# Performance work log

Measured on AMD Instinct MI355X. Metric: run time of the kernel, lower is better.

The kernel has to match this reference:

```python
import jax, jax.numpy as jnp
import numpy as np

N_NODES = 50000


def _sage_conv(x, src, dst, Wl, bl, Wr):
    # PyG SAGEConv (mean aggr): out = lin_l(mean_{j in N(i)} x_j) + lin_r(x_i)
    msgs = x[src]                                              # [E, F]
    agg = jax.ops.segment_sum(msgs, dst, num_segments=N_NODES)  # [N, F]
    cnt = jax.ops.segment_sum(jnp.ones((dst.shape[0],), x.dtype), dst,
                              num_segments=N_NODES)
    mean = agg / jnp.maximum(cnt, 1.0)[:, None]
    return mean @ Wl + bl + x @ Wr


def setup_inputs() -> dict:
    key = jax.random.key(0)
    ks = jax.random.split(key, 12)
    in_c, hid_c, out_c = 128, 128, 64
    E, P = 800000, 200000
    s = lambda k, shp: jax.random.normal(k, shp, dtype=jnp.float32) * (1.0 / np.sqrt(shp[0]))
    return {
        "x": jax.random.normal(ks[0], (N_NODES, in_c), dtype=jnp.float32),
        "edge_index": jax.random.randint(ks[1], (2, E), 0, N_NODES),
        "edge_pairs": jax.random.randint(ks[2], (2, P), 0, N_NODES),
        "W1l": s(ks[3], (in_c, hid_c)),
        "b1": jnp.zeros((hid_c,), jnp.float32),
        "W1r": s(ks[4], (in_c, hid_c)),
        "W2l": s(ks[5], (hid_c, out_c)),
        "b2": jnp.zeros((out_c,), jnp.float32),
        "W2r": s(ks[6], (hid_c, out_c)),
        "Wlin": s(ks[7], (2 * out_c, 1)),
        "blin": jnp.zeros((1,), jnp.float32),
    }


def reference(x, edge_index, edge_pairs, W1l, b1, W1r, W2l, b2, W2r, Wlin, blin):
    src, dst = edge_index[0], edge_index[1]
    h = jax.nn.relu(_sage_conv(x, src, dst, W1l, b1, W1r))
    z = _sage_conv(h, src, dst, W2l, b2, W2r)                 # [N, out_c]
    ps, pd = edge_pairs[0], edge_pairs[1]
    hcat = jnp.concatenate([z[ps], z[pd]], axis=1)            # [P, 2*out_c]
    logits = hcat @ Wlin + blin                               # [P, 1]
    return jax.nn.sigmoid(logits).reshape(-1)
```

## Files before the change

kernel.cpp:

```cpp
#include <hip/hip_runtime.h>
#include <math.h>


typedef __attribute__((ext_vector_type(8))) short bf16x8;
typedef __attribute__((ext_vector_type(4))) float f32x4;
typedef unsigned int uint32;
typedef unsigned short ushort16;

#define MAXBUCK 784
#define NHB 512

__device__ __forceinline__ ushort16 f2bf(float f) {
    uint32 u = __float_as_uint(f);
    uint32 r = u + 0x7FFFu + ((u >> 16) & 1u);
    return (ushort16)(r >> 16);
}


__global__ __launch_bounds__(256)
void prep_kernel(const float* __restrict__ x, uint32* __restrict__ xh, long long n4,
                 const float* __restrict__ W1l, const float* __restrict__ W1r,
                 ushort16* __restrict__ W1t,
                 const float* __restrict__ W2l, const float* __restrict__ W2r,
                 const float* __restrict__ Wlin, const float* __restrict__ b2,
                 float* __restrict__ fw, float* __restrict__ fc,
                 const int* __restrict__ dst, int* __restrict__ hcnt, int E,
                 int nbx, int nbw1) {
    __shared__ int lh[MAXBUCK];
    int b = blockIdx.x;
    int t = threadIdx.x;
    if (b < nbx) {
        long long i = (long long)b * 256 + t;
        if (i < n4) {
            float4 v = ((const float4*)x)[i];
            uint2 o;
            o.x = (uint32)f2bf(v.x) | ((uint32)f2bf(v.y) << 16);
            o.y = (uint32)f2bf(v.z) | ((uint32)f2bf(v.w) << 16);
            ((uint2*)xh)[i] = o;
        }
    } else if (b < nbx + nbw1) {
        int idx = (b - nbx) * 256 + t;
        int n = idx >> 8, k = idx & 255;
        float v = (k < 128) ? W1l[k * 128 + n] : W1r[(k - 128) * 128 + n];
        W1t[n * 256 + k] = f2bf(v);
    } else if (b == nbx + nbw1) {
        if (t < 128) {
            float a = 0.f, c = 0.f;
            for (int l = 0; l < 64; ++l) {
                float w = W2l[t * 64 + l];
                a += w * Wlin[l];
                c += w * Wlin[64 + l];
            }
            fw[t] = a; fw[128 + t] = c;
        } else {
            int k = t - 128;
            float a = 0.f, c = 0.f;
            for (int l = 0; l < 64; ++l) {
                float w = W2r[k * 64 + l];
                a += w * Wlin[l];
                c += w * Wlin[64 + l];
            }
            fw[256 + k] = a; fw[384 + k] = c;
        }
        if (t == 0) { float s = 0.f; for (int l = 0; l < 64; ++l) s += b2[l] * Wlin[l];      fc[0] = s; }
        if (t == 1) { float s = 0.f; for (int l = 0; l < 64; ++l) s += b2[l] * Wlin[64 + l]; fc[1] = s; }
    } else {
        int hb = b - nbx - nbw1 - 1;
        for (int i = t; i < MAXBUCK; i += 256) lh[i] = 0;
        __syncthreads();
        int per = (E + NHB - 1) / NHB;
        int e0 = hb * per, e1 = min(e0 + per, E);
        for (int e = e0 + t; e < e1; e += 256) atomicAdd(&lh[dst[e] >> 6], 1);
        __syncthreads();
        for (int i = t; i < MAXBUCK; i += 256)
            hcnt[hb * MAXBUCK + i] = lh[i];
    }
}


__global__ __launch_bounds__(256)
void offs_kernel(const int* __restrict__ hcnt, int* __restrict__ boff,
                 int* __restrict__ tot) {
    int k = blockIdx.x * 4 + (threadIdx.x >> 6);
    int lane = threadIdx.x & 63;
    if (k >= MAXBUCK) return;
    int carry = 0;
    #pragma unroll
    for (int c = 0; c < NHB / 64; ++c) {
        int hb = c * 64 + lane;
        int v = hcnt[hb * MAXBUCK + k];
        int s = v;
        #pragma unroll
        for (int off = 1; off < 64; off <<= 1) {
            int u = __shfl_up(s, off, 64);
            if (lane >= off) s += u;
        }
        boff[hb * MAXBUCK + k] = carry + s - v;
        carry += __shfl(s, 63, 64);
    }
    if (lane == 0) tot[k] = carry;
}


__global__ void bucket_scan_kernel(const int* __restrict__ tot,
                                   int* __restrict__ bbase, int nbuck) {
    __shared__ int part[256];
    int t = threadIdx.x;
    int lo = t * 4;
    int hi = min(lo + 4, nbuck);
    int loc[4];
    int s = 0;
    for (int i = lo; i < hi; ++i) { loc[i - lo] = tot[i]; s += loc[i - lo]; }
    part[t] = s;
    __syncthreads();
    for (int off = 1; off < 256; off <<= 1) {
        int v = (t >= off) ? part[t - off] : 0;
        __syncthreads();
        part[t] += v;
        __syncthreads();
    }
    int run = (t == 0) ? 0 : part[t - 1];
    for (int i = lo; i < hi; ++i) { bbase[i] = run; run += loc[i - lo]; }
    if (t == 255) bbase[nbuck] = part[255];
}


__global__ __launch_bounds__(256)
void scatter_kernel(const int* __restrict__ src, const int* __restrict__ dst,
                    const int* __restrict__ bbase, const int* __restrict__ boff,
                    uint32* __restrict__ recs, int E) {
    __shared__ int lh[MAXBUCK];
    __shared__ int lb[MAXBUCK];
    int t = threadIdx.x;
    int hb = blockIdx.x;
    int per = (E + NHB - 1) / NHB;
    int e0 = hb * per, e1 = min(e0 + per, E);
    for (int i = t; i < MAXBUCK; i += 256) {
        lh[i] = 0;
        lb[i] = bbase[i] + boff[hb * MAXBUCK + i];
    }
    __syncthreads();
    for (int e = e0 + t; e < e1; e += 256) {
        int d = dst[e];
        int b = d >> 6;
        int r = atomicAdd(&lh[b], 1);
        recs[lb[b] + r] = (uint32)src[e] | ((uint32)(d & 63) << 16);
    }
}


__global__ __launch_bounds__(256)
void sort_kernel(const uint32* __restrict__ recs, const int* __restrict__ bbase,
                 int* __restrict__ rowptr, ushort16* __restrict__ esrc,
                 int N, int E) {
    __shared__ int lh[64];
    int b = blockIdx.x;
    int t = threadIdx.x;
    int s0 = bbase[b], s1 = bbase[b + 1];
    if (t < 64) lh[t] = 0;
    __syncthreads();
    for (int i = s0 + t; i < s1; i += 256)
        atomicAdd(&lh[recs[i] >> 16], 1);
    __syncthreads();
    if (t < 64) {
        int v = lh[t];
        int incl = v;
        #pragma unroll
        for (int off = 1; off < 64; off <<= 1) {
            int u = __shfl_up(incl, off, 64);
            if (t >= off) incl += u;
        }
        int excl = incl - v;
        int node = b * 64 + t;
        if (node < N) rowptr[node] = s0 + excl;
        lh[t] = excl;
    }
    __syncthreads();
    for (int i = s0 + t; i < s1; i += 256) {
        uint32 r = recs[i];
        int pos = atomicAdd(&lh[r >> 16], 1);
        esrc[s0 + pos] = (ushort16)(r & 0xFFFFu);
    }
    if (b == 0 && t == 0) rowptr[N] = E;
}


__global__ void agg_mean_x_kernel(const uint32* __restrict__ xh,
                                  const int* __restrict__ rowptr,
                                  const ushort16* __restrict__ esrc,
                                  uint32* __restrict__ meanh, int N) {
    int node = blockIdx.x * 4 + (threadIdx.x >> 6);
    int lane = threadIdx.x & 63;
    if (node >= N) return;
    int s0 = rowptr[node], s1 = rowptr[node + 1];
    if (s0 == s1) { meanh[(size_t)node * 64 + lane] = 0u; return; }
    float ax[16] = {}, ay[16] = {};
    for (int k = s0; k < s1; k += 16) {
        int idx[16]; float msk[16];
        #pragma unroll
        for (int j = 0; j < 16; ++j) {
            int kj = k + j;
            idx[j] = esrc[kj < s1 ? kj : k];
            msk[j] = (kj < s1) ? 1.f : 0.f;
        }
        #pragma unroll
        for (int j = 0; j < 16; ++j) {
            uint32 v = xh[(size_t)idx[j] * 64 + lane];
            ax[j] += __uint_as_float(v << 16) * msk[j];
            ay[j] += __uint_as_float(v & 0xFFFF0000u) * msk[j];
        }
    }
    float sx = 0.f, sy = 0.f;
    #pragma unroll
    for (int j = 0; j < 16; ++j) { sx += ax[j]; sy += ay[j]; }
    float inv = 1.0f / (float)(s1 - s0);
    meanh[(size_t)node * 64 + lane] = (uint32)f2bf(sx * inv) | ((uint32)f2bf(sy * inv) << 16);
}


__global__ __launch_bounds__(256)
void gemm1_mfma_kernel(const ushort16* __restrict__ meanh,
                       const ushort16* __restrict__ xh,
                       const ushort16* __restrict__ W1t,
                       const float* __restrict__ b1,
                       const float* __restrict__ fw,
                       float2* __restrict__ pab, float2* __restrict__ quv, int N) {
    int wave = threadIdx.x >> 6;
    int lane = threadIdx.x & 63;
    int m = lane & 15;
    int quad = lane >> 4;
    int row0 = blockIdx.x * 64 + wave * 16;
    int arow = row0 + m; if (arow > N - 1) arow = N - 1;
    f32x4 acc[8];
    #pragma unroll
    for (int c = 0; c < 8; ++c) acc[c] = (f32x4){0.f, 0.f, 0.f, 0.f};
    #pragma unroll
    for (int ks = 0; ks < 8; ++ks) {
        int k0 = ks * 32;
        const ushort16* Ab = (ks < 4) ? meanh : xh;
        bf16x8 a = *(const bf16x8*)(Ab + (size_t)arow * 128 + (k0 & 127) + quad * 8);
        #pragma unroll
        for (int c = 0; c < 8; ++c) {
            bf16x8 b = *(const bf16x8*)(W1t + (size_t)(c * 16 + m) * 256 + k0 + quad * 8);
            acc[c] = __builtin_amdgcn_mfma_f32_16x16x32_bf16(a, b, acc[c], 0, 0, 0);
        }
    }
    float da[4] = {}, dc[4] = {}, db[4] = {}, dd[4] = {};
    #pragma unroll
    for (int c = 0; c < 8; ++c) {
        int col = c * 16 + m;
        float bias = b1[col];
        float wa = fw[col], wc = fw[128 + col], wb = fw[256 + col], wd = fw[384 + col];
        #pragma unroll
        for (int r = 0; r < 4; ++r) {
            float v = fmaxf(acc[c][r] + bias, 0.f);
            da[r] += v * wa; dc[r] += v * wc; db[r] += v * wb; dd[r] += v * wd;
        }
    }
    #pragma unroll
    for (int r = 0; r < 4; ++r) {
        #pragma unroll
        for (int msk = 1; msk < 16; msk <<= 1) {
            da[r] += __shfl_xor(da[r], msk, 64);
            dc[r] += __shfl_xor(dc[r], msk, 64);
            db[r] += __shfl_xor(db[r], msk, 64);
            dd[r] += __shfl_xor(dd[r], msk, 64);
        }
    }
    if (m == 0) {
        #pragma unroll
        for (int r = 0; r < 4; ++r) {
            int grow = row0 + quad * 4 + r;
            if (grow < N) {
                pab[grow] = make_float2(da[r], dc[r]);
                quv[grow] = make_float2(db[r], dd[r]);
            }
        }
    }
}


__global__ void agg_link_kernel(const float2* __restrict__ pab,
                                const float2* __restrict__ quv,
                                const int* __restrict__ rowptr,
                                const ushort16* __restrict__ esrc,
                                const float* __restrict__ fc,
                                float* __restrict__ za, float* __restrict__ zb, int N) {
    int i = blockIdx.x * blockDim.x + threadIdx.x;
    if (i >= N) return;
    int s0 = rowptr[i], s1 = rowptr[i + 1];
    float a[8] = {}, c[8] = {};
    for (int k = s0; k < s1; k += 8) {
        int idx[8]; float msk[8];
        #pragma unroll
        for (int j = 0; j < 8; ++j) {
            int kj = k + j;
            idx[j] = esrc[kj < s1 ? kj : k];
            msk[j] = (kj < s1) ? 1.f : 0.f;
        }
        #pragma unroll
        for (int j = 0; j < 8; ++j) {
            float2 p = pab[idx[j]];
            a[j] += p.x * msk[j];
            c[j] += p.y * msk[j];
        }
    }
    float spa = 0.f, spc = 0.f;
    #pragma unroll
    for (int j = 0; j < 8; ++j) { spa += a[j]; spc += c[j]; }
    float inv = (s1 > s0) ? 1.0f / (float)(s1 - s0) : 0.f;
    float2 q = quv[i];
    za[i] = spa * inv + q.x + fc[0];
    zb[i] = spc * inv + q.y + fc[1];
}


__global__ void link_kernel(const float* __restrict__ za, const float* __restrict__ zb,
                            const int* __restrict__ ps, const int* __restrict__ pd,
                            const float* __restrict__ blin,
                            float* __restrict__ out, int P) {
    int p = blockIdx.x * blockDim.x + threadIdx.x;
    if (p >= P) return;
    float logit = za[ps[p]] + zb[pd[p]] + blin[0];
    out[p] = 1.0f / (1.0f + expf(-logit));
}


extern "C" void kernel_launch(void* const* d_in, const int* in_sizes, int n_in,
                              void* d_out, int out_size, void* d_ws, size_t ws_size,
                              hipStream_t stream) {
    const float* x          = (const float*)d_in[0];
    const int*   edge_index = (const int*)d_in[1];
    const int*   edge_pairs = (const int*)d_in[2];
    const float* W1l        = (const float*)d_in[3];
    const float* b1         = (const float*)d_in[4];
    const float* W1r        = (const float*)d_in[5];
    const float* W2l        = (const float*)d_in[6];
    const float* b2         = (const float*)d_in[7];
    const float* W2r        = (const float*)d_in[8];
    const float* Wlin       = (const float*)d_in[9];
    const float* blin       = (const float*)d_in[10];
    float* out = (float*)d_out;

    const int N = in_sizes[0] / 128;
    const int E = in_sizes[1] / 2;
    const int P = in_sizes[2] / 2;
    const int NBUCK = (N + 63) >> 6;

    const int* src = edge_index;
    const int* dst = edge_index + E;
    const int* ps  = edge_pairs;
    const int* pd  = edge_pairs + P;

    ushort16* xh    = (ushort16*)d_ws;
    ushort16* meanh = xh + (size_t)N * 128;
    ushort16* W1t   = meanh + (size_t)N * 128;
    float* fw      = (float*)(W1t + 128 * 256);
    float* fc      = fw + 512;
    float2* pab    = (float2*)(fc + 4);
    float2* quv    = pab + N;
    float* za      = (float*)(quv + N);
    float* zb      = za + N;
    int* bbase     = (int*)(zb + N);
    int* tot       = bbase + (MAXBUCK + 16);
    int* hcnt      = tot + MAXBUCK;
    int* boff      = hcnt + NHB * MAXBUCK;
    int* rowptr    = boff + NHB * MAXBUCK;
    uint32* recs   = (uint32*)(rowptr + N + 16);
    ushort16* esrc = (ushort16*)(recs + E);

    const long long n4 = (long long)N * 128 / 4;
    const int nbx  = (int)((n4 + 255) / 256);
    const int nbw1 = 128;

    prep_kernel<<<nbx + nbw1 + 1 + NHB, 256, 0, stream>>>(
        x, (uint32*)xh, n4, W1l, W1r, W1t, W2l, W2r, Wlin, b2, fw, fc,
        dst, hcnt, E, nbx, nbw1);

    offs_kernel<<<MAXBUCK / 4, 256, 0, stream>>>(hcnt, boff, tot);
    bucket_scan_kernel<<<1, 256, 0, stream>>>(tot, bbase, NBUCK);
    scatter_kernel<<<NHB, 256, 0, stream>>>(src, dst, bbase, boff, recs, E);
    sort_kernel<<<NBUCK, 256, 0, stream>>>(recs, bbase, rowptr, esrc, N, E);

    agg_mean_x_kernel<<<(N + 3) / 4, 256, 0, stream>>>((const uint32*)xh, rowptr, esrc,
                                                       (uint32*)meanh, N);
    gemm1_mfma_kernel<<<(N + 63) / 64, 256, 0, stream>>>(meanh, xh, W1t, b1, fw,
                                                         pab, quv, N);

    agg_link_kernel<<<(N + 255) / 256, 256, 0, stream>>>(pab, quv, rowptr, esrc, fc,
                                                         za, zb, N);

    link_kernel<<<(P + 255) / 256, 256, 0, stream>>>(za, zb, ps, pd, blin, out, P);
}
```

Measured before the change: 200.7 us.

## Fuse bucket sort, mean aggregation and first GEMM into one kernel

Merges sort_kernel, agg_mean_x_kernel and gemm1_mfma_kernel into a single per-bucket kernel. The sorted edge sources are staged in shared memory, the 64 node means are computed into an LDS tile, and that tile feeds the MFMA directly, so the meanh global round-trip and two launches go away. In exchange, aggregation parallelism drops to 782 blocks with each wave looping over 16 nodes serially, which may reduce latency hiding for the gather. LDS use also grows, which can lower occupancy.

```diff
diff --git a/kernel.cpp b/kernel.cpp
--- a/kernel.cpp
+++ b/kernel.cpp
@@ -9,6 +9,8 @@
 
 #define MAXBUCK 784
 #define NHB 512
+#define CAP 2048
+#define MHS 68
 
 __device__ __forceinline__ ushort16 f2bf(float f) {
     uint32 u = __float_as_uint(f);
@@ -150,10 +152,16 @@
 
 
 __global__ __launch_bounds__(256)
-void sort_kernel(const uint32* __restrict__ recs, const int* __restrict__ bbase,
-                 int* __restrict__ rowptr, ushort16* __restrict__ esrc,
-                 int N, int E) {
+void mega_kernel(const uint32* __restrict__ xh_u, const ushort16* __restrict__ xh,
+                 const ushort16* __restrict__ W1t,
+                 const uint32* __restrict__ recs, const int* __restrict__ bbase,
+                 int* __restrict__ rowptr, ushort16* __restrict__ esrc_g,
+                 const float* __restrict__ b1, const float* __restrict__ fw,
+                 float2* __restrict__ pab, float2* __restrict__ quv, int N, int E) {
     __shared__ int lh[64];
+    __shared__ int st_[64];
+    __shared__ unsigned short es[CAP];
+    __shared__ uint32 mh[64 * MHS];
     int b = blockIdx.x;
     int t = threadIdx.x;
     int s0 = bbase[b], s1 = bbase[b + 1];
@@ -173,63 +181,58 @@
         int excl = incl - v;
         int node = b * 64 + t;
         if (node < N) rowptr[node] = s0 + excl;
+        st_[t] = excl;
         lh[t] = excl;
     }
+    if (b == 0 && t == 0) rowptr[N] = E;
     __syncthreads();
     for (int i = s0 + t; i < s1; i += 256) {
         uint32 r = recs[i];
         int pos = atomicAdd(&lh[r >> 16], 1);
-        esrc[s0 + pos] = (ushort16)(r & 0xFFFFu);
-    }
-    if (b == 0 && t == 0) rowptr[N] = E;
-}
-
-
-__global__ void agg_mean_x_kernel(const uint32* __restrict__ xh,
-                                  const int* __restrict__ rowptr,
-                                  const ushort16* __restrict__ esrc,
-                                  uint32* __restrict__ meanh, int N) {
-    int node = blockIdx.x * 4 + (threadIdx.x >> 6);
-    int lane = threadIdx.x & 63;
-    if (node >= N) return;
-    int s0 = rowptr[node], s1 = rowptr[node + 1];
-    if (s0 == s1) { meanh[(size_t)node * 64 + lane] = 0u; return; }
-    float ax[16] = {}, ay[16] = {};
-    for (int k = s0; k < s1; k += 16) {
-        int idx[16]; float msk[16];
-        #pragma unroll
-        for (int j = 0; j < 16; ++j) {
-            int kj = k + j;
-            idx[j] = esrc[kj < s1 ? kj : k];
-            msk[j] = (kj < s1) ? 1.f : 0.f;
-        }
-        #pragma unroll
-        for (int j = 0; j < 16; ++j) {
-            uint32 v = xh[(size_t)idx[j] * 64 + lane];
-            ax[j] += __uint_as_float(v << 16) * msk[j];
-            ay[j] += __uint_as_float(v & 0xFFFF0000u) * msk[j];
-        }
-    }
-    float sx = 0.f, sy = 0.f;
-    #pragma unroll
-    for (int j = 0; j < 16; ++j) { sx += ax[j]; sy += ay[j]; }
-    float inv = 1.0f / (float)(s1 - s0);
-    meanh[(size_t)node * 64 + lane] = (uint32)f2bf(sx * inv) | ((uint32)f2bf(sy * inv) << 16);
-}
-
-
-__global__ __launch_bounds__(256)
-void gemm1_mfma_kernel(const ushort16* __restrict__ meanh,
-                       const ushort16* __restrict__ xh,
-                       const ushort16* __restrict__ W1t,
-                       const float* __restrict__ b1,
-                       const float* __restrict__ fw,
-                       float2* __restrict__ pab, float2* __restrict__ quv, int N) {
-    int wave = threadIdx.x >> 6;
-    int lane = threadIdx.x & 63;
+        unsigned short sv = (unsigned short)(r & 0xFFFFu);
+        if (pos < CAP) es[pos] = sv;
+        ((unsigned short*)esrc_g)[s0 + pos] = sv;
+    }
+    if (s1 - s0 > CAP) __threadfence();
+    __syncthreads();
+
+    int wave = t >> 6, lane = t & 63;
+
+    for (int rr = 0; rr < 16; ++rr) {
+        int n = wave * 16 + rr;
+        int e0 = st_[n], e1 = lh[n];
+        if (e0 == e1) { mh[n * MHS + lane] = 0u; continue; }
+        float ax[16] = {}, ay[16] = {};
+        for (int k = e0; k < e1; k += 16) {
+            int idx[16]; float msk[16];
+            #pragma unroll
+            for (int j = 0; j < 16; ++j) {
+                int kj = k + j;
+                int ksel = kj < e1 ? kj : e0;
+                int v;
+                if (ksel < CAP) v = es[ksel];
+                else v = ((const unsigned short*)esrc_g)[s0 + ksel];
+                idx[j] = v;
+                msk[j] = (kj < e1) ? 1.f : 0.f;
+            }
+            #pragma unroll
+            for (int j = 0; j < 16; ++j) {
+                uint32 v = xh_u[(size_t)idx[j] * 64 + lane];
+                ax[j] += __uint_as_float(v << 16) * msk[j];
+                ay[j] += __uint_as_float(v & 0xFFFF0000u) * msk[j];
+            }
+        }
+        float sx = 0.f, sy = 0.f;
+        #pragma unroll
+        for (int j = 0; j < 16; ++j) { sx += ax[j]; sy += ay[j]; }
+        float inv = 1.0f / (float)(e1 - e0);
+        mh[n * MHS + lane] = (uint32)f2bf(sx * inv) | ((uint32)f2bf(sy * inv) << 16);
+    }
+    __syncthreads();
+
     int m = lane & 15;
     int quad = lane >> 4;
-    int row0 = blockIdx.x * 64 + wave * 16;
+    int row0 = b * 64 + wave * 16;
     int arow = row0 + m; if (arow > N - 1) arow = N - 1;
     f32x4 acc[8];
     #pragma unroll
@@ -237,12 +240,15 @@
     #pragma unroll
     for (int ks = 0; ks < 8; ++ks) {
         int k0 = ks * 32;
-        const ushort16* Ab = (ks < 4) ? meanh : xh;
-        bf16x8 a = *(const bf16x8*)(Ab + (size_t)arow * 128 + (k0 & 127) + quad * 8);
+        bf16x8 a;
+        if (ks < 4)
+            a = *(const bf16x8*)&mh[(size_t)(wave * 16 + m) * MHS + ks * 16 + quad * 4];
+        else
+            a = *(const bf16x8*)(xh + (size_t)arow * 128 + (k0 - 128) + quad * 8);
         #pragma unroll
         for (int c = 0; c < 8; ++c) {
-            bf16x8 b = *(const bf16x8*)(W1t + (size_t)(c * 16 + m) * 256 + k0 + quad * 8);
-            acc[c] = __builtin_amdgcn_mfma_f32_16x16x32_bf16(a, b, acc[c], 0, 0, 0);
+            bf16x8 bfr = *(const bf16x8*)(W1t + (size_t)(c * 16 + m) * 256 + k0 + quad * 8);
+            acc[c] = __builtin_amdgcn_mfma_f32_16x16x32_bf16(a, bfr, acc[c], 0, 0, 0);
         }
     }
     float da[4] = {}, dc[4] = {}, db[4] = {}, dd[4] = {};
@@ -353,8 +359,7 @@
     const int* pd  = edge_pairs + P;
 
     ushort16* xh    = (ushort16*)d_ws;
-    ushort16* meanh = xh + (size_t)N * 128;
-    ushort16* W1t   = meanh + (size_t)N * 128;
+    ushort16* W1t   = xh + (size_t)N * 128;
     float* fw      = (float*)(W1t + 128 * 256);
     float* fc      = fw + 512;
     float2* pab    = (float2*)(fc + 4);
@@ -380,12 +385,9 @@
     offs_kernel<<<MAXBUCK / 4, 256, 0, stream>>>(hcnt, boff, tot);
     bucket_scan_kernel<<<1, 256, 0, stream>>>(tot, bbase, NBUCK);
     scatter_kernel<<<NHB, 256, 0, stream>>>(src, dst, bbase, boff, recs, E);
-    sort_kernel<<<NBUCK, 256, 0, stream>>>(recs, bbase, rowptr, esrc, N, E);
-
-    agg_mean_x_kernel<<<(N + 3) / 4, 256, 0, stream>>>((const uint32*)xh, rowptr, esrc,
-                                                       (uint32*)meanh, N);
-    gemm1_mfma_kernel<<<(N + 63) / 64, 256, 0, stream>>>(meanh, xh, W1t, b1, fw,
-                                                         pab, quv, N);
+
+    mega_kernel<<<NBUCK, 256, 0, stream>>>((const uint32*)xh, xh, W1t, recs, bbase,
+                                           rowptr, esrc, b1, fw, pab, quv, N, E);
 
     agg_link_kernel<<<(N + 255) / 256, 256, 0, stream>>>(pab, quv, rowptr, esrc, fc,
                                                          za, zb, N);
```

Measured after the change: 223.0 us. +11.1%, slower.

## Split neighbor aggregation across lane groups with 16-byte gathers and shuffle reductions

Applied to the files above, without the earlier changes.

The first-layer mean aggregation now splits each wave into four 16-lane groups. Each group gathers a different neighbor's full row with 16-byte uint4 loads into 8 accumulators, and the groups are combined with xor shuffles, so a wave has several neighbor rows in flight with fewer load instructions. The second aggregation kernel now uses four threads per node instead of one, with a shuffle reduction, which is meant to cut per-thread serial latency on high-degree nodes. The cost is extra shuffles, idle lanes for low-degree nodes, and a launch four times larger for the link aggregation.

```diff
diff --git a/kernel.cpp b/kernel.cpp
--- a/kernel.cpp
+++ b/kernel.cpp
@@ -185,36 +185,58 @@
 }
 
 
-__global__ void agg_mean_x_kernel(const uint32* __restrict__ xh,
-                                  const int* __restrict__ rowptr,
-                                  const ushort16* __restrict__ esrc,
-                                  uint32* __restrict__ meanh, int N) {
+__global__ __launch_bounds__(256)
+void agg_mean_x_kernel(const uint32* __restrict__ xh,
+                       const int* __restrict__ rowptr,
+                       const ushort16* __restrict__ esrc,
+                       uint32* __restrict__ meanh, int N) {
     int node = blockIdx.x * 4 + (threadIdx.x >> 6);
     int lane = threadIdx.x & 63;
     if (node >= N) return;
     int s0 = rowptr[node], s1 = rowptr[node + 1];
-    if (s0 == s1) { meanh[(size_t)node * 64 + lane] = 0u; return; }
-    float ax[16] = {}, ay[16] = {};
+    int q = lane >> 4;
+    int w = lane & 15;
+    if (s0 == s1) {
+        if (q == 0) ((uint4*)meanh)[(size_t)node * 16 + w] = make_uint4(0u, 0u, 0u, 0u);
+        return;
+    }
+    float acc[8] = {};
     for (int k = s0; k < s1; k += 16) {
-        int idx[16]; float msk[16];
-        #pragma unroll
-        for (int j = 0; j < 16; ++j) {
-            int kj = k + j;
-            idx[j] = esrc[kj < s1 ? kj : k];
-            msk[j] = (kj < s1) ? 1.f : 0.f;
-        }
-        #pragma unroll
-        for (int j = 0; j < 16; ++j) {
-            uint32 v = xh[(size_t)idx[j] * 64 + lane];
-            ax[j] += __uint_as_float(v << 16) * msk[j];
-            ay[j] += __uint_as_float(v & 0xFFFF0000u) * msk[j];
-        }
-    }
-    float sx = 0.f, sy = 0.f;
-    #pragma unroll
-    for (int j = 0; j < 16; ++j) { sx += ax[j]; sy += ay[j]; }
-    float inv = 1.0f / (float)(s1 - s0);
-    meanh[(size_t)node * 64 + lane] = (uint32)f2bf(sx * inv) | ((uint32)f2bf(sy * inv) << 16);
+        int e[4]; int idx[4]; float msk[4];
+        #pragma unroll
+        for (int j = 0; j < 4; ++j) {
+            e[j] = k + q * 4 + j;
+            int valid = e[j] < s1;
+            idx[j] = esrc[valid ? e[j] : s0];
+            msk[j] = valid ? 1.f : 0.f;
+        }
+        #pragma unroll
+        for (int j = 0; j < 4; ++j) {
+            uint4 v = ((const uint4*)xh)[(size_t)idx[j] * 16 + w];
+            acc[0] += __uint_as_float(v.x << 16) * msk[j];
+            acc[1] += __uint_as_float(v.x & 0xFFFF0000u) * msk[j];
+            acc[2] += __uint_as_float(v.y << 16) * msk[j];
+            acc[3] += __uint_as_float(v.y & 0xFFFF0000u) * msk[j];
+            acc[4] += __uint_as_float(v.z << 16) * msk[j];
+            acc[5] += __uint_as_float(v.z & 0xFFFF0000u) * msk[j];
+            acc[6] += __uint_as_float(v.w << 16) * msk[j];
+            acc[7] += __uint_as_float(v.w & 0xFFFF0000u) * msk[j];
+        }
+    }
+    #pragma unroll
+    for (int i = 0; i < 8; ++i) {
+        acc[i] += __shfl_xor(acc[i], 16, 64);
+        acc[i] += __shfl_xor(acc[i], 32, 64);
+    }
+    if (q == 0) {
+        float inv = 1.0f / (float)(s1 - s0);
+        uint4 o;
+        o.x = (uint32)f2bf(acc[0] * inv) | ((uint32)f2bf(acc[1] * inv) << 16);
+        o.y = (uint32)f2bf(acc[2] * inv) | ((uint32)f2bf(acc[3] * inv) << 16);
+        o.z = (uint32)f2bf(acc[4] * inv) | ((uint32)f2bf(acc[5] * inv) << 16);
+        o.w = (uint32)f2bf(acc[6] * inv) | ((uint32)f2bf(acc[7] * inv) << 16);
+        ((uint4*)meanh)[(size_t)node * 16 + w] = o;
+    }
 }
 
 
@@ -280,38 +302,39 @@
 }
 
 
-__global__ void agg_link_kernel(const float2* __restrict__ pab,
-                                const float2* __restrict__ quv,
-                                const int* __restrict__ rowptr,
-                                const ushort16* __restrict__ esrc,
-                                const float* __restrict__ fc,
-                                float* __restrict__ za, float* __restrict__ zb, int N) {
-    int i = blockIdx.x * blockDim.x + threadIdx.x;
+__global__ __launch_bounds__(256)
+void agg_link_kernel(const float2* __restrict__ pab,
+                     const float2* __restrict__ quv,
+                     const int* __restrict__ rowptr,
+                     const ushort16* __restrict__ esrc,
+                     const float* __restrict__ fc,
+                     float* __restrict__ za, float* __restrict__ zb, int N) {
+    int gi = blockIdx.x * blockDim.x + threadIdx.x;
+    int i = gi >> 2;
+    int q = gi & 3;
     if (i >= N) return;
     int s0 = rowptr[i], s1 = rowptr[i + 1];
-    float a[8] = {}, c[8] = {};
-    for (int k = s0; k < s1; k += 8) {
-        int idx[8]; float msk[8];
-        #pragma unroll
-        for (int j = 0; j < 8; ++j) {
-            int kj = k + j;
-            idx[j] = esrc[kj < s1 ? kj : k];
-            msk[j] = (kj < s1) ? 1.f : 0.f;
-        }
-        #pragma unroll
-        for (int j = 0; j < 8; ++j) {
-            float2 p = pab[idx[j]];
-            a[j] += p.x * msk[j];
-            c[j] += p.y * msk[j];
-        }
-    }
-    float spa = 0.f, spc = 0.f;
-    #pragma unroll
-    for (int j = 0; j < 8; ++j) { spa += a[j]; spc += c[j]; }
-    float inv = (s1 > s0) ? 1.0f / (float)(s1 - s0) : 0.f;
-    float2 q = quv[i];
-    za[i] = spa * inv + q.x + fc[0];
-    zb[i] = spc * inv + q.y + fc[1];
+    float a0 = 0.f, c0 = 0.f, a1 = 0.f, c1 = 0.f;
+    for (int k = s0 + q; k < s1; k += 8) {
+        int kB = k + 4;
+        int vB = kB < s1;
+        int idxA = esrc[k];
+        int idxB = esrc[vB ? kB : k];
+        float2 pA = pab[idxA];
+        float2 pB = pab[idxB];
+        float mB = vB ? 1.f : 0.f;
+        a0 += pA.x; c0 += pA.y;
+        a1 += pB.x * mB; c1 += pB.y * mB;
+    }
+    float spa = a0 + a1, spc = c0 + c1;
+    spa += __shfl_xor(spa, 1, 64); spa += __shfl_xor(spa, 2, 64);
+    spc += __shfl_xor(spc, 1, 64); spc += __shfl_xor(spc, 2, 64);
+    if (q == 0) {
+        float inv = (s1 > s0) ? 1.0f / (float)(s1 - s0) : 0.f;
+        float2 qv = quv[i];
+        za[i] = spa * inv + qv.x + fc[0];
+        zb[i] = spc * inv + qv.y + fc[1];
+    }
 }
 
 
@@ -387,8 +410,8 @@
     gemm1_mfma_kernel<<<(N + 63) / 64, 256, 0, stream>>>(meanh, xh, W1t, b1, fw,
                                                          pab, quv, N);
 
-    agg_link_kernel<<<(N + 255) / 256, 256, 0, stream>>>(pab, quv, rowptr, esrc, fc,
-                                                         za, zb, N);
+    agg_link_kernel<<<(4 * N + 255) / 256, 256, 0, stream>>>(pab, quv, rowptr, esrc, fc,
+                                                             za, zb, N);
 
     link_kernel<<<(P + 255) / 256, 256, 0, stream>>>(za, zb, ps, pd, blin, out, P);
 }
```

Result: faster. 195.3 us (-2.7%).
